# Performance work log

Measured on AMD Instinct MI355X. Metric: run time of the kernel, lower is better.

Reference implementation:

```python
import jax, jax.numpy as jnp
import numpy as np

NUM_HEADS = 8
LN_EPS = 1e-5


def _layernorm(x, g, b):
    m = jnp.mean(x, axis=-1, keepdims=True)
    v = jnp.mean(jnp.square(x - m), axis=-1, keepdims=True)
    return (x - m) * jax.lax.rsqrt(v + LN_EPS) * g + b


def setup_inputs() -> dict:
    key = jax.random.key(0)
    ks = jax.random.split(key, 10)
    D, C, Cin = 2, 256, 64  # depth, embed dim, input channels
    w = lambda k, shape: jax.random.normal(k, shape, jnp.float32) * 0.02
    return {
        "x": jax.random.normal(ks[0], (4, Cin, 12, 12, 12), jnp.float32),
        "W_pe": w(ks[1], (Cin, C)),
        "b_pe": jnp.zeros((C,), jnp.float32),
        "cls_token": w(ks[2], (1, 1, C)),
        "ln1_g": jnp.ones((D, C), jnp.float32),
        "ln1_b": jnp.zeros((D, C), jnp.float32),
        "Wqkv": w(ks[3], (D, C, 3 * C)),
        "Wproj": w(ks[4], (D, C, C)),
        "bproj": jnp.zeros((D, C), jnp.float32),
        "ln2_g": jnp.ones((D, C), jnp.float32),
        "ln2_b": jnp.zeros((D, C), jnp.float32),
        "W1": w(ks[5], (D, C, C)),
        "b1": jnp.zeros((D, C), jnp.float32),
        "W2": w(ks[6], (D, C, C)),
        "b2": jnp.zeros((D, C), jnp.float32),
        "normf_g": jnp.ones((C,), jnp.float32),
        "normf_b": jnp.zeros((C,), jnp.float32),
    }


def reference(x, W_pe, b_pe, cls_token, ln1_g, ln1_b, Wqkv, Wproj, bproj,
              ln2_g, ln2_b, W1, b1, W2, b2, normf_g, normf_b):
    B, Cin, H, W, L = x.shape
    C = W_pe.shape[1]
    hd = C // NUM_HEADS
    scale = hd ** (-0.5)

    # PatchEmbed: 1x1x1 Conv3d == per-voxel linear projection, then flatten to tokens
    tok = jnp.einsum('bchwl,cd->bhwld', x, W_pe).reshape(B, H * W * L, C) + b_pe
    cls = jnp.broadcast_to(cls_token, (B, 1, C))
    t = jnp.concatenate([cls, tok], axis=1)  # [B, N, C], N = H*W*L + 1
    N = t.shape[1]

    depth = Wqkv.shape[0]
    for i in range(depth):
        # --- self-attention ---
        y = _layernorm(t, ln1_g[i], ln1_b[i])
        qkv = (y @ Wqkv[i]).reshape(B, N, 3, NUM_HEADS, hd)
        qkv = jnp.transpose(qkv, (2, 0, 3, 1, 4))  # [3, B, H, N, hd]
        q, k, v = qkv[0], qkv[1], qkv[2]
        attn = jnp.einsum('bhnd,bhmd->bhnm', q, k) * scale
        attn = jax.nn.softmax(attn, axis=-1)
        o = jnp.einsum('bhnm,bhmd->bhnd', attn, v)
        o = jnp.transpose(o, (0, 2, 1, 3)).reshape(B, N, C)
        t = t + (o @ Wproj[i] + bproj[i])
        # --- MLP (mlp_ratio=1.0, exact GELU) ---
        y = _layernorm(t, ln2_g[i], ln2_b[i])
        h = jax.nn.gelu(y @ W1[i] + b1[i], approximate=False)
        t = t + (h @ W2[i] + b2[i])

    t = _layernorm(t, normf_g, normf_b)
    x_cls = t[:, 0]                                   # [B, C]
    feat = t[:, 1:]                                   # [B, H*W*L, C]
    feat = jnp.transpose(feat, (0, 2, 1)).reshape(B, C, H, W, L)  # downsample = Identity for dim=256
    return x_cls, feat
```

## Files before the change

kernel.cpp:

```cpp
#include <hip/hip_runtime.h>
#include <hip/hip_bf16.h>
#include <math.h>

#define B_   4
#define CIN  64
#define P_   1728
#define N_   1729
#define C_   256
#define NH_  8
#define HD_  32
#define M_   (B_*N_)
#define NPAD 1792

typedef __bf16 bf16x8 __attribute__((ext_vector_type(8)));
typedef __bf16 bf16x4 __attribute__((ext_vector_type(4)));
typedef float  f32x4  __attribute__((ext_vector_type(4)));
typedef float  f32x16 __attribute__((ext_vector_type(16)));

__global__ __launch_bounds__(256) void embed2(
    const float* __restrict__ x, const float* __restrict__ Wpe,
    const float* __restrict__ bpe, const float* __restrict__ cls,
    float* __restrict__ t)
{
    int idx = blockIdx.x*256 + threadIdx.x;
    int c   = idx & 255;
    int n   = (idx >> 8) % N_;
    int b   = idx / (N_*256);
    if (n == 0) { t[idx] = cls[c]; return; }
    int p = n - 1;
    float acc = bpe[c];
    for (int ci = 0; ci < CIN; ++ci)
        acc += x[(size_t)(b*CIN + ci)*P_ + p] * Wpe[ci*C_ + c];
    t[idx] = acc;
}

__global__ __launch_bounds__(256) void ln4(
    const float* __restrict__ in, __bf16* __restrict__ out,
    const float* __restrict__ g, const float* __restrict__ bb)
{
    int wv = threadIdx.x >> 6, lane = threadIdx.x & 63;
    size_t row = (size_t)blockIdx.x*4 + wv;
    float4 v = *(const float4*)&in[row*C_ + lane*4];
    float s1 = (v.x+v.y)+(v.z+v.w);
    float s2 = (v.x*v.x+v.y*v.y)+(v.z*v.z+v.w*v.w);
    #pragma unroll
    for (int off = 32; off >= 1; off >>= 1) {
        s1 += __shfl_xor(s1, off);
        s2 += __shfl_xor(s2, off);
    }
    float mean = s1*(1.0f/C_);
    float var  = fmaxf(s2*(1.0f/C_) - mean*mean, 0.0f);
    float rstd = rsqrtf(var + 1e-5f);
    float4 gg = *(const float4*)&g[lane*4];
    float4 bv = *(const float4*)&bb[lane*4];
    bf16x4 r;
    r[0] = (__bf16)((v.x-mean)*rstd*gg.x + bv.x);
    r[1] = (__bf16)((v.y-mean)*rstd*gg.y + bv.y);
    r[2] = (__bf16)((v.z-mean)*rstd*gg.z + bv.z);
    r[3] = (__bf16)((v.w-mean)*rstd*gg.w + bv.w);
    *(bf16x4*)&out[row*C_ + lane*4] = r;
}

__global__ __launch_bounds__(256) void ln4f(
    const float* __restrict__ in, float* __restrict__ out,
    const float* __restrict__ g, const float* __restrict__ bb,
    float* __restrict__ cls_out)
{
    int wv = threadIdx.x >> 6, lane = threadIdx.x & 63;
    size_t row = (size_t)blockIdx.x*4 + wv;
    float4 v = *(const float4*)&in[row*C_ + lane*4];
    float s1 = (v.x+v.y)+(v.z+v.w);
    float s2 = (v.x*v.x+v.y*v.y)+(v.z*v.z+v.w*v.w);
    #pragma unroll
    for (int off = 32; off >= 1; off >>= 1) {
        s1 += __shfl_xor(s1, off);
        s2 += __shfl_xor(s2, off);
    }
    float mean = s1*(1.0f/C_);
    float var  = fmaxf(s2*(1.0f/C_) - mean*mean, 0.0f);
    float rstd = rsqrtf(var + 1e-5f);
    float4 gg = *(const float4*)&g[lane*4];
    float4 bv = *(const float4*)&bb[lane*4];
    float4 r;
    r.x = (v.x-mean)*rstd*gg.x + bv.x;
    r.y = (v.y-mean)*rstd*gg.y + bv.y;
    r.z = (v.z-mean)*rstd*gg.z + bv.z;
    r.w = (v.w-mean)*rstd*gg.w + bv.w;
    *(float4*)&out[row*C_ + lane*4] = r;
    if ((row % N_) == 0)
        *(float4*)&cls_out[(row / N_)*C_ + lane*4] = r;
}

__global__ __launch_bounds__(256) void wprep2(
    const float* __restrict__ Wqkv, const float* __restrict__ Wproj,
    const float* __restrict__ W1,   const float* __restrict__ W2,
    __bf16* __restrict__ wT)
{
    int z = blockIdx.z, which = z >> 1, layer = z & 1;
    const float* src; __bf16* dst; int NC;
    if (which == 0) {
        src = Wqkv + (size_t)layer*C_*768;
        dst = wT   + (size_t)layer*768*256;
        NC  = 768;
    } else {
        NC = 256;
        const float* b3 = (which == 1) ? Wproj : (which == 2) ? W1 : W2;
        src = b3 + (size_t)layer*65536;
        dst = wT + 2*768*256 + (size_t)((which-1)*2 + layer)*65536;
    }
    int n0 = blockIdx.x*32; if (n0 >= NC) return;
    int k0 = blockIdx.y*32;
    __shared__ float tile[32][33];
    int c = threadIdx.x & 31, r = threadIdx.x >> 5;
    for (int rr = r; rr < 32; rr += 8)
        tile[rr][c] = src[(size_t)(k0+rr)*NC + n0 + c];
    __syncthreads();
    for (int rr = r; rr < 32; rr += 8)
        dst[(size_t)(n0+rr)*256 + k0 + c] = (__bf16)tile[c][rr];
}

__global__ __launch_bounds__(256) void padzero(
    __bf16* __restrict__ kB, __bf16* __restrict__ vB)
{
    int idx = blockIdx.x*256 + threadIdx.x;
    if (idx >= 32*63*32) return;
    int d  = idx & 31;
    int n  = (idx >> 5) % 63 + N_;
    int bh = idx / (63*32);
    kB[((size_t)bh*NPAD + n)*32 + d] = (__bf16)0.f;
    vB[((size_t)bh*32 + d)*NPAD + n] = (__bf16)0.f;
}

template<int NC, bool ADD, bool GELU, bool BIAS, bool OUTBF>
__global__ __launch_bounds__(256) void gemm4(
    const __bf16* __restrict__ A, const __bf16* __restrict__ Wt,
    const float* __restrict__ bias, float* __restrict__ outF,
    __bf16* __restrict__ outB)
{
    __shared__ __align__(16) __bf16 As[2][64*64];
    __shared__ __align__(16) __bf16 Bs[2][64*64];
    int r0 = blockIdx.x*64, c0 = blockIdx.y*64;
    int tid = threadIdx.x;
    int wv = tid >> 6, lane = tid & 63, quad = lane >> 4, mn = lane & 15;
    int sr = tid >> 2, sc = tid & 3;
    int ga = r0 + sr; if (ga >= M_) ga = M_ - 1;

    f32x4 acc[4];
    #pragma unroll
    for (int ct = 0; ct < 4; ++ct)
        #pragma unroll
        for (int rr = 0; rr < 4; ++rr) acc[ct][rr] = 0.f;

    bf16x8 ra0, ra1, rb0, rb1;
#define GLOAD(KC) do {                                                   \
        ra0 = *(const bf16x8*)&A[(size_t)ga*256 + (KC)*64 + sc*8];       \
        ra1 = *(const bf16x8*)&A[(size_t)ga*256 + (KC)*64 + sc*8 + 32];  \
        rb0 = *(const bf16x8*)&Wt[(size_t)(c0+sr)*256 + (KC)*64 + sc*8]; \
        rb1 = *(const bf16x8*)&Wt[(size_t)(c0+sr)*256 + (KC)*64 + sc*8 + 32]; \
    } while (0)
#define SSTORE(BUF) do {                                                 \
        *(bf16x8*)&As[BUF][sr*64 + ((sc ^ (sr & 7))*8)]       = ra0;     \
        *(bf16x8*)&As[BUF][sr*64 + (((sc+4) ^ (sr & 7))*8)]   = ra1;     \
        *(bf16x8*)&Bs[BUF][sr*64 + ((sc ^ (sr & 7))*8)]       = rb0;     \
        *(bf16x8*)&Bs[BUF][sr*64 + (((sc+4) ^ (sr & 7))*8)]   = rb1;     \
    } while (0)

    GLOAD(0);
    SSTORE(0);
    __syncthreads();

    for (int kc = 0; kc < 4; ++kc) {
        int cur = kc & 1;
        if (kc < 3) GLOAD(kc+1);
        __builtin_amdgcn_sched_barrier(0);

        #pragma unroll
        for (int h = 0; h < 2; ++h) {
            bf16x8 a = *(const bf16x8*)&As[cur][(wv*16 + mn)*64 + (((h*4+quad) ^ (mn & 7))*8)];
            #pragma unroll
            for (int ct = 0; ct < 4; ++ct) {
                bf16x8 b = *(const bf16x8*)&Bs[cur][(ct*16 + mn)*64 + (((h*4+quad) ^ (mn & 7))*8)];
                acc[ct] = __builtin_amdgcn_mfma_f32_16x16x32_bf16(a, b, acc[ct], 0, 0, 0);
            }
        }

        if (kc < 3) {
            SSTORE(cur^1);
            __syncthreads();
        }
    }
#undef GLOAD
#undef SSTORE

    #pragma unroll
    for (int ct = 0; ct < 4; ++ct) {
        int col = c0 + ct*16 + mn;
        #pragma unroll
        for (int rr = 0; rr < 4; ++rr) {
            int row = r0 + wv*16 + quad*4 + rr;
            if (row >= M_) continue;
            float val = acc[ct][rr];
            if (BIAS) val += bias[col];
            if (GELU) val = 0.5f*val*(1.f + erff(val*0.70710678118654752f));
            size_t oi = (size_t)row*NC + col;
            if (OUTBF) outB[oi] = (__bf16)val;
            else if (ADD) outF[oi] += val;
            else outF[oi] = val;
        }
    }
}

__global__ __launch_bounds__(256) void gemm_qkv4(
    const __bf16* __restrict__ A, const __bf16* __restrict__ Wt,
    __bf16* __restrict__ qB, __bf16* __restrict__ kB, __bf16* __restrict__ vB)
{
    __shared__ __align__(16) __bf16 As[2][64*64];
    __shared__ __align__(16) __bf16 Bs[2][64*64];
    int r0 = blockIdx.x*64, c0 = blockIdx.y*64;
    int tid = threadIdx.x;
    int wv = tid >> 6, lane = tid & 63, quad = lane >> 4, mn = lane & 15;
    int sr = tid >> 2, sc = tid & 3;
    int ga = r0 + sr; if (ga >= M_) ga = M_ - 1;

    f32x4 acc[4];
    #pragma unroll
    for (int ct = 0; ct < 4; ++ct)
        #pragma unroll
        for (int rr = 0; rr < 4; ++rr) acc[ct][rr] = 0.f;

    bf16x8 ra0, ra1, rb0, rb1;
#define GLOAD(KC) do {                                                   \
        ra0 = *(const bf16x8*)&A[(size_t)ga*256 + (KC)*64 + sc*8];       \
        ra1 = *(const bf16x8*)&A[(size_t)ga*256 + (KC)*64 + sc*8 + 32];  \
        rb0 = *(const bf16x8*)&Wt[(size_t)(c0+sr)*256 + (KC)*64 + sc*8]; \
        rb1 = *(const bf16x8*)&Wt[(size_t)(c0+sr)*256 + (KC)*64 + sc*8 + 32]; \
    } while (0)
#define SSTORE(BUF) do {                                                 \
        *(bf16x8*)&As[BUF][sr*64 + ((sc ^ (sr & 7))*8)]       = ra0;     \
        *(bf16x8*)&As[BUF][sr*64 + (((sc+4) ^ (sr & 7))*8)]   = ra1;     \
        *(bf16x8*)&Bs[BUF][sr*64 + ((sc ^ (sr & 7))*8)]       = rb0;     \
        *(bf16x8*)&Bs[BUF][sr*64 + (((sc+4) ^ (sr & 7))*8)]   = rb1;     \
    } while (0)

    GLOAD(0);
    SSTORE(0);
    __syncthreads();

    for (int kc = 0; kc < 4; ++kc) {
        int cur = kc & 1;
        if (kc < 3) GLOAD(kc+1);
        __builtin_amdgcn_sched_barrier(0);

        #pragma unroll
        for (int h = 0; h < 2; ++h) {
            bf16x8 a = *(const bf16x8*)&As[cur][(wv*16 + mn)*64 + (((h*4+quad) ^ (mn & 7))*8)];
            #pragma unroll
            for (int ct = 0; ct < 4; ++ct) {
                bf16x8 b = *(const bf16x8*)&Bs[cur][(ct*16 + mn)*64 + (((h*4+quad) ^ (mn & 7))*8)];
                acc[ct] = __builtin_amdgcn_mfma_f32_16x16x32_bf16(a, b, acc[ct], 0, 0, 0);
            }
        }

        if (kc < 3) {
            SSTORE(cur^1);
            __syncthreads();
        }
    }
#undef GLOAD
#undef SSTORE

    const float scale = 0.2550348727f;
    #pragma unroll
    for (int ct = 0; ct < 4; ++ct) {
        int col = c0 + ct*16 + mn;
        #pragma unroll
        for (int rr = 0; rr < 4; ++rr) {
            int row = r0 + wv*16 + quad*4 + rr;
            if (row >= M_) continue;
            int b = row / N_, n = row - b*N_;
            float val = acc[ct][rr];
            if (col < 256) {
                int h = col >> 5, dd = col & 31;
                qB[((size_t)(b*NH_+h)*NPAD + n)*32 + dd] = (__bf16)(val*scale);
            } else if (col < 512) {
                int h = (col-256) >> 5, dd = col & 31;
                kB[((size_t)(b*NH_+h)*NPAD + n)*32 + dd] = (__bf16)val;
            } else {
                int h = (col-512) >> 5, dd = col & 31;
                vB[((size_t)(b*NH_+h)*32 + dd)*NPAD + n] = (__bf16)val;
            }
        }
    }
}

__device__ __forceinline__ float fexp2(float x) {
    float r; asm("v_exp_f32 %0, %1" : "=v"(r) : "v"(x)); return r;
}
__device__ __forceinline__ unsigned cvtpk_bf16(float lo, float hi) {
    unsigned r;
    asm("v_cvt_pk_bf16_f32 %0, %1, %2" : "=v"(r) : "v"(lo), "v"(hi));
    return r;
}

__global__ __launch_bounds__(128) void attn14(
    const __bf16* __restrict__ qB, const __bf16* __restrict__ kB,
    const __bf16* __restrict__ vB, __bf16* __restrict__ o)
{
    int bh = blockIdx.x, b = bh >> 3, h = bh & 7;
    int q0 = blockIdx.y * 64;
    int tid = threadIdx.x;
    int wv = tid >> 6, lane = tid & 63, lo5 = lane & 31, hi = lane >> 5;

    const __bf16* kbase = kB + (size_t)bh*NPAD*32;
    const __bf16* vbase = vB + (size_t)bh*32*NPAD;

    const __bf16* qrow = qB + ((size_t)bh*NPAD + q0 + wv*32 + lo5)*32 + hi*8;
    bf16x8 qf0 = *(const bf16x8*)(qrow);
    bf16x8 qf1 = *(const bf16x8*)(qrow + 16);

    f32x16 oaccA, oaccB;
    #pragma unroll
    for (int r = 0; r < 16; ++r) { oaccA[r] = 0.f; oaccB[r] = 0.f; }
    float lsum = 0.f;

    const __bf16* kp = kbase + (size_t)lo5*32 + hi*8;
    const __bf16* vp = vbase + (size_t)lo5*NPAD + hi*8;

    for (int t = 0; t < 14; ++t) {
        bf16x8 kf0[4], kf1[4], vf0[4], vf1[4];
        #pragma unroll
        for (int kg = 0; kg < 4; ++kg) {
            const __bf16* kpp = kp + (size_t)t*128*32 + kg*32*32;
            kf0[kg] = *(const bf16x8*)(kpp);
            kf1[kg] = *(const bf16x8*)(kpp + 16);
            const __bf16* vpp = vp + (size_t)t*128 + kg*32;
            vf0[kg] = *(const bf16x8*)(vpp);
            vf1[kg] = *(const bf16x8*)(vpp + 16);
        }

        #pragma unroll
        for (int kg = 0; kg < 4; ++kg) {
            f32x16 s;
            #pragma unroll
            for (int r = 0; r < 16; ++r) s[r] = 0.f;
            __builtin_amdgcn_s_setprio(1);
            s = __builtin_amdgcn_mfma_f32_32x32x16_bf16(kf0[kg], qf0, s, 0, 0, 0);
            s = __builtin_amdgcn_mfma_f32_32x32x16_bf16(kf1[kg], qf1, s, 0, 0, 0);
            __builtin_amdgcn_s_setprio(0);

            float p[16];
            #pragma unroll
            for (int r = 0; r < 16; ++r) p[r] = fexp2(s[r]);
            float l0 = 0.f, l1 = 0.f;
            #pragma unroll
            for (int r = 0; r < 8; ++r) { l0 += p[r]; l1 += p[r+8]; }
            lsum += l0 + l1;

            unsigned a0 = cvtpk_bf16(p[0],  p[1]),  a1 = cvtpk_bf16(p[2],  p[3]);
            unsigned b0 = cvtpk_bf16(p[4],  p[5]),  b1 = cvtpk_bf16(p[6],  p[7]);
            unsigned c0 = cvtpk_bf16(p[8],  p[9]),  c1 = cvtpk_bf16(p[10], p[11]);
            unsigned d0 = cvtpk_bf16(p[12], p[13]), d1 = cvtpk_bf16(p[14], p[15]);
            asm("v_permlane32_swap_b32 %0, %1" : "+v"(a0), "+v"(b0));
            asm("v_permlane32_swap_b32 %0, %1" : "+v"(a1), "+v"(b1));
            asm("v_permlane32_swap_b32 %0, %1" : "+v"(c0), "+v"(d0));
            asm("v_permlane32_swap_b32 %0, %1" : "+v"(c1), "+v"(d1));
            union { bf16x8 v; unsigned u[4]; } f0, f1;
            f0.u[0] = a0; f0.u[1] = a1; f0.u[2] = b0; f0.u[3] = b1;
            f1.u[0] = c0; f1.u[1] = c1; f1.u[2] = d0; f1.u[3] = d1;

            __builtin_amdgcn_s_setprio(1);
            if (kg & 1) {
                oaccB = __builtin_amdgcn_mfma_f32_32x32x16_bf16(f0.v, vf0[kg], oaccB, 0, 0, 0);
                oaccB = __builtin_amdgcn_mfma_f32_32x32x16_bf16(f1.v, vf1[kg], oaccB, 0, 0, 0);
            } else {
                oaccA = __builtin_amdgcn_mfma_f32_32x32x16_bf16(f0.v, vf0[kg], oaccA, 0, 0, 0);
                oaccA = __builtin_amdgcn_mfma_f32_32x32x16_bf16(f1.v, vf1[kg], oaccA, 0, 0, 0);
            }
            __builtin_amdgcn_s_setprio(0);
        }
    }

    lsum += __shfl_xor(lsum, 32);
    float inv = 1.0f / (lsum - 63.0f);

    #pragma unroll
    for (int r = 0; r < 16; ++r) {
        float oa = oaccA[r] + oaccB[r];
        int qrw = (r & 3) + 8*(r >> 2) + 4*hi;
        float li = __shfl(inv, qrw);
        int q = q0 + wv*32 + qrw;
        if (q < N_)
            o[((size_t)b*N_ + q)*C_ + h*HD_ + lo5] = (__bf16)(oa * li);
    }
}

__global__ __launch_bounds__(256) void feat3(
    const float* __restrict__ y, float* __restrict__ outf)
{
    __shared__ float tl[32][33];
    int p0 = blockIdx.x*32, c0 = blockIdx.y*32, b = blockIdx.z;
    int cc = threadIdx.x & 31, rr = threadIdx.x >> 5;
    for (int i = rr; i < 32; i += 8)
        tl[i][cc] = y[((size_t)(b*N_) + 1 + p0 + i)*C_ + c0 + cc];
    __syncthreads();
    for (int i = rr; i < 32; i += 8)
        outf[((size_t)(b*C_) + c0 + i)*P_ + p0 + cc] = tl[cc][i];
}

extern "C" void kernel_launch(void* const* d_in, const int* in_sizes, int n_in,
                              void* d_out, int out_size, void* d_ws, size_t ws_size,
                              hipStream_t stream)
{
    const float* x        = (const float*)d_in[0];
    const float* W_pe     = (const float*)d_in[1];
    const float* b_pe     = (const float*)d_in[2];
    const float* cls_tok  = (const float*)d_in[3];
    const float* ln1_g    = (const float*)d_in[4];
    const float* ln1_b    = (const float*)d_in[5];
    const float* Wqkv     = (const float*)d_in[6];
    const float* Wproj    = (const float*)d_in[7];
    const float* bproj    = (const float*)d_in[8];
    const float* ln2_g    = (const float*)d_in[9];
    const float* ln2_b    = (const float*)d_in[10];
    const float* W1       = (const float*)d_in[11];
    const float* b1       = (const float*)d_in[12];
    const float* W2       = (const float*)d_in[13];
    const float* b2       = (const float*)d_in[14];
    const float* normf_g  = (const float*)d_in[15];
    const float* normf_b  = (const float*)d_in[16];

    const size_t MC = (size_t)M_*C_;
    float*  ws  = (float*)d_ws;
    float*  t   = ws;
    float*  yf  = ws + MC;
    __bf16* ybf = (__bf16*)(ws + 2*MC);
    __bf16* hbf = (__bf16*)(ws + 2*MC + MC/2);
    __bf16* obf = (__bf16*)(ws + 2*MC + MC);
    __bf16* wT  = (__bf16*)(ws + 2*MC + 3*(MC/2));
    __bf16* qB  = wT + 2*768*256 + 6*256*256;
    __bf16* kB  = qB + (size_t)B_*NH_*NPAD*32;
    __bf16* vB  = kB + (size_t)B_*NH_*NPAD*32;

    __bf16* projT = wT + 2*768*256;
    __bf16* w1T   = projT + 2*256*256;
    __bf16* w2T   = w1T   + 2*256*256;

    float* out_cls  = (float*)d_out;
    float* out_feat = out_cls + B_*C_;

    wprep2<<<dim3(24, 8, 8), 256, 0, stream>>>(Wqkv, Wproj, W1, W2, wT);
    padzero<<<252, 256, 0, stream>>>(kB, vB);
    embed2<<<(B_*N_*C_)/256, 256, 0, stream>>>(x, W_pe, b_pe, cls_tok, t);

    const int GRID_M = (M_ + 63) / 64;
    for (int i = 0; i < 2; ++i) {
        ln4<<<M_/4, 256, 0, stream>>>(t, ybf, ln1_g + i*C_, ln1_b + i*C_);
        gemm_qkv4<<<dim3(GRID_M, 12), 256, 0, stream>>>(
            ybf, wT + (size_t)i*768*256, qB, kB, vB);
        attn14<<<dim3(32, 28), 128, 0, stream>>>(qB, kB, vB, obf);
        gemm4<256,true,false,true,false><<<dim3(GRID_M, 4), 256, 0, stream>>>(
            obf, projT + (size_t)i*65536, bproj + i*C_, t, nullptr);
        ln4<<<M_/4, 256, 0, stream>>>(t, ybf, ln2_g + i*C_, ln2_b + i*C_);
        gemm4<256,false,true,true,true><<<dim3(GRID_M, 4), 256, 0, stream>>>(
            ybf, w1T + (size_t)i*65536, b1 + i*C_, nullptr, hbf);
        gemm4<256,true,false,true,false><<<dim3(GRID_M, 4), 256, 0, stream>>>(
            hbf, w2T + (size_t)i*65536, b2 + i*C_, t, nullptr);
    }

    ln4f<<<M_/4, 256, 0, stream>>>(t, yf, normf_g, normf_b, out_cls);
    feat3<<<dim3(54, 8, 4), 256, 0, stream>>>(yf, out_feat);
}
```

Before: 307.7 us.

## Split attention KV range across two wave pairs and merge partials in LDS

Doubles the attention block to four waves. Each pair of waves handles half of the key/value sequence (896 keys each) for the same 64 queries, and the partial outputs and row sums are combined through shared memory before normalization. The inner loop is also restructured into a software-pipelined loop that prefetches the next 32-key K/V fragments one step ahead, replacing the batched loads of four groups. This is meant to raise wave-level parallelism and hide load latency, at the cost of an LDS reduction, a block-wide barrier, and idle waves during the epilogue.

```diff
diff --git a/kernel.cpp b/kernel.cpp
--- a/kernel.cpp
+++ b/kernel.cpp
@@ -302,19 +302,25 @@
     return r;
 }
 
-__global__ __launch_bounds__(128) void attn14(
+__global__ __launch_bounds__(256) void attn15(
     const __bf16* __restrict__ qB, const __bf16* __restrict__ kB,
     const __bf16* __restrict__ vB, __bf16* __restrict__ o)
 {
     int bh = blockIdx.x, b = bh >> 3, h = bh & 7;
     int q0 = blockIdx.y * 64;
     int tid = threadIdx.x;
-    int wv = tid >> 6, lane = tid & 63, lo5 = lane & 31, hi = lane >> 5;
+    int wv = tid >> 6;
+    int qw  = wv & 1;
+    int swv = wv >> 1;
+    int lane = tid & 63, lo5 = lane & 31, hi = lane >> 5;
+
+    __shared__ float lds_o[2][16][64];
+    __shared__ float lds_l[2][64];
 
     const __bf16* kbase = kB + (size_t)bh*NPAD*32;
     const __bf16* vbase = vB + (size_t)bh*32*NPAD;
 
-    const __bf16* qrow = qB + ((size_t)bh*NPAD + q0 + wv*32 + lo5)*32 + hi*8;
+    const __bf16* qrow = qB + ((size_t)bh*NPAD + q0 + qw*32 + lo5)*32 + hi*8;
     bf16x8 qf0 = *(const bf16x8*)(qrow);
     bf16x8 qf1 = *(const bf16x8*)(qrow + 16);
 
@@ -323,74 +329,89 @@
     for (int r = 0; r < 16; ++r) { oaccA[r] = 0.f; oaccB[r] = 0.f; }
     float lsum = 0.f;
 
-    const __bf16* kp = kbase + (size_t)lo5*32 + hi*8;
-    const __bf16* vp = vbase + (size_t)lo5*NPAD + hi*8;
-
-    for (int t = 0; t < 14; ++t) {
-        bf16x8 kf0[4], kf1[4], vf0[4], vf1[4];
-        #pragma unroll
-        for (int kg = 0; kg < 4; ++kg) {
-            const __bf16* kpp = kp + (size_t)t*128*32 + kg*32*32;
-            kf0[kg] = *(const bf16x8*)(kpp);
-            kf1[kg] = *(const bf16x8*)(kpp + 16);
-            const __bf16* vpp = vp + (size_t)t*128 + kg*32;
-            vf0[kg] = *(const bf16x8*)(vpp);
-            vf1[kg] = *(const bf16x8*)(vpp + 16);
-        }
-
-        #pragma unroll
-        for (int kg = 0; kg < 4; ++kg) {
-            f32x16 s;
-            #pragma unroll
-            for (int r = 0; r < 16; ++r) s[r] = 0.f;
-            __builtin_amdgcn_s_setprio(1);
-            s = __builtin_amdgcn_mfma_f32_32x32x16_bf16(kf0[kg], qf0, s, 0, 0, 0);
-            s = __builtin_amdgcn_mfma_f32_32x32x16_bf16(kf1[kg], qf1, s, 0, 0, 0);
-            __builtin_amdgcn_s_setprio(0);
-
-            float p[16];
-            #pragma unroll
-            for (int r = 0; r < 16; ++r) p[r] = fexp2(s[r]);
-            float l0 = 0.f, l1 = 0.f;
-            #pragma unroll
-            for (int r = 0; r < 8; ++r) { l0 += p[r]; l1 += p[r+8]; }
-            lsum += l0 + l1;
-
-            unsigned a0 = cvtpk_bf16(p[0],  p[1]),  a1 = cvtpk_bf16(p[2],  p[3]);
-            unsigned b0 = cvtpk_bf16(p[4],  p[5]),  b1 = cvtpk_bf16(p[6],  p[7]);
-            unsigned c0 = cvtpk_bf16(p[8],  p[9]),  c1 = cvtpk_bf16(p[10], p[11]);
-            unsigned d0 = cvtpk_bf16(p[12], p[13]), d1 = cvtpk_bf16(p[14], p[15]);
-            asm("v_permlane32_swap_b32 %0, %1" : "+v"(a0), "+v"(b0));
-            asm("v_permlane32_swap_b32 %0, %1" : "+v"(a1), "+v"(b1));
-            asm("v_permlane32_swap_b32 %0, %1" : "+v"(c0), "+v"(d0));
-            asm("v_permlane32_swap_b32 %0, %1" : "+v"(c1), "+v"(d1));
-            union { bf16x8 v; unsigned u[4]; } f0, f1;
-            f0.u[0] = a0; f0.u[1] = a1; f0.u[2] = b0; f0.u[3] = b1;
-            f1.u[0] = c0; f1.u[1] = c1; f1.u[2] = d0; f1.u[3] = d1;
-
-            __builtin_amdgcn_s_setprio(1);
-            if (kg & 1) {
-                oaccB = __builtin_amdgcn_mfma_f32_32x32x16_bf16(f0.v, vf0[kg], oaccB, 0, 0, 0);
-                oaccB = __builtin_amdgcn_mfma_f32_32x32x16_bf16(f1.v, vf1[kg], oaccB, 0, 0, 0);
-            } else {
-                oaccA = __builtin_amdgcn_mfma_f32_32x32x16_bf16(f0.v, vf0[kg], oaccA, 0, 0, 0);
-                oaccA = __builtin_amdgcn_mfma_f32_32x32x16_bf16(f1.v, vf1[kg], oaccA, 0, 0, 0);
-            }
-            __builtin_amdgcn_s_setprio(0);
-        }
+    const __bf16* kp = kbase + (size_t)(swv*896 + lo5)*32 + hi*8;
+    const __bf16* vp = vbase + (size_t)lo5*NPAD + swv*896 + hi*8;
+
+    bf16x8 kf0n = *(const bf16x8*)(kp);
+    bf16x8 kf1n = *(const bf16x8*)(kp + 16);
+    bf16x8 vf0n = *(const bf16x8*)(vp);
+    bf16x8 vf1n = *(const bf16x8*)(vp + 16);
+
+    for (int i = 0; i < 28; ++i) {
+        bf16x8 kf0 = kf0n, kf1 = kf1n, vf0 = vf0n, vf1 = vf1n;
+        if (i < 27) {
+            const __bf16* kpp = kp + (size_t)(i+1)*1024;
+            kf0n = *(const bf16x8*)(kpp);
+            kf1n = *(const bf16x8*)(kpp + 16);
+            const __bf16* vpp = vp + (i+1)*32;
+            vf0n = *(const bf16x8*)(vpp);
+            vf1n = *(const bf16x8*)(vpp + 16);
+        }
+        __builtin_amdgcn_sched_barrier(0);
+
+        f32x16 s;
+        #pragma unroll
+        for (int r = 0; r < 16; ++r) s[r] = 0.f;
+        __builtin_amdgcn_s_setprio(1);
+        s = __builtin_amdgcn_mfma_f32_32x32x16_bf16(kf0, qf0, s, 0, 0, 0);
+        s = __builtin_amdgcn_mfma_f32_32x32x16_bf16(kf1, qf1, s, 0, 0, 0);
+        __builtin_amdgcn_s_setprio(0);
+
+        float p[16];
+        #pragma unroll
+        for (int r = 0; r < 16; ++r) p[r] = fexp2(s[r]);
+        float l0 = 0.f, l1 = 0.f;
+        #pragma unroll
+        for (int r = 0; r < 8; ++r) { l0 += p[r]; l1 += p[r+8]; }
+        lsum += l0 + l1;
+
+        unsigned a0 = cvtpk_bf16(p[0],  p[1]),  a1 = cvtpk_bf16(p[2],  p[3]);
+        unsigned b0 = cvtpk_bf16(p[4],  p[5]),  b1 = cvtpk_bf16(p[6],  p[7]);
+        unsigned c0 = cvtpk_bf16(p[8],  p[9]),  c1 = cvtpk_bf16(p[10], p[11]);
+        unsigned d0 = cvtpk_bf16(p[12], p[13]), d1 = cvtpk_bf16(p[14], p[15]);
+        asm("v_permlane32_swap_b32 %0, %1" : "+v"(a0), "+v"(b0));
+        asm("v_permlane32_swap_b32 %0, %1" : "+v"(a1), "+v"(b1));
+        asm("v_permlane32_swap_b32 %0, %1" : "+v"(c0), "+v"(d0));
+        asm("v_permlane32_swap_b32 %0, %1" : "+v"(c1), "+v"(d1));
+        union { bf16x8 v; unsigned u[4]; } f0, f1;
+        f0.u[0] = a0; f0.u[1] = a1; f0.u[2] = b0; f0.u[3] = b1;
+        f1.u[0] = c0; f1.u[1] = c1; f1.u[2] = d0; f1.u[3] = d1;
+
+        __builtin_amdgcn_s_setprio(1);
+        if (i & 1) {
+            oaccB = __builtin_amdgcn_mfma_f32_32x32x16_bf16(f0.v, vf0, oaccB, 0, 0, 0);
+            oaccB = __builtin_amdgcn_mfma_f32_32x32x16_bf16(f1.v, vf1, oaccB, 0, 0, 0);
+        } else {
+            oaccA = __builtin_amdgcn_mfma_f32_32x32x16_bf16(f0.v, vf0, oaccA, 0, 0, 0);
+            oaccA = __builtin_amdgcn_mfma_f32_32x32x16_bf16(f1.v, vf1, oaccA, 0, 0, 0);
+        }
+        __builtin_amdgcn_s_setprio(0);
     }
 
     lsum += __shfl_xor(lsum, 32);
-    float inv = 1.0f / (lsum - 63.0f);
-
-    #pragma unroll
-    for (int r = 0; r < 16; ++r) {
-        float oa = oaccA[r] + oaccB[r];
-        int qrw = (r & 3) + 8*(r >> 2) + 4*hi;
-        float li = __shfl(inv, qrw);
-        int q = q0 + wv*32 + qrw;
-        if (q < N_)
-            o[((size_t)b*N_ + q)*C_ + h*HD_ + lo5] = (__bf16)(oa * li);
+
+    f32x16 oa;
+    #pragma unroll
+    for (int r = 0; r < 16; ++r) oa[r] = oaccA[r] + oaccB[r];
+
+    if (swv == 1) {
+        #pragma unroll
+        for (int r = 0; r < 16; ++r) lds_o[qw][r][lane] = oa[r];
+        lds_l[qw][lane] = lsum;
+    }
+    __syncthreads();
+    if (swv == 0) {
+        float lother = lds_l[qw][lane];
+        float inv = 1.0f / (lsum + lother - 63.0f);
+        #pragma unroll
+        for (int r = 0; r < 16; ++r) {
+            float ov = oa[r] + lds_o[qw][r][lane];
+            int qrw = (r & 3) + 8*(r >> 2) + 4*hi;
+            float li = __shfl(inv, qrw);
+            int q = q0 + qw*32 + qrw;
+            if (q < N_)
+                o[((size_t)b*N_ + q)*C_ + h*HD_ + lo5] = (__bf16)(ov * li);
+        }
     }
 }
 
@@ -457,7 +478,7 @@
         ln4<<<M_/4, 256, 0, stream>>>(t, ybf, ln1_g + i*C_, ln1_b + i*C_);
         gemm_qkv4<<<dim3(GRID_M, 12), 256, 0, stream>>>(
             ybf, wT + (size_t)i*768*256, qB, kB, vB);
-        attn14<<<dim3(32, 28), 128, 0, stream>>>(qB, kB, vB, obf);
+        attn15<<<dim3(32, 28), 256, 0, stream>>>(qB, kB, vB, obf);
         gemm4<256,true,false,true,false><<<dim3(GRID_M, 4), 256, 0, stream>>>(
             obf, projT + (size_t)i*65536, bproj + i*C_, t, nullptr);
         ln4<<<M_/4, 256, 0, stream>>>(t, ybf, ln2_g + i*C_, ln2_b + i*C_);
```

New measurement: 304.6 us. No clear change (-1.0%).
